# Kernel optimization log

Hardware: AMD Instinct MI355X
Metric: run time of the kernel (lower is better)

The kernel has to match this reference:

```python
import jax, jax.numpy as jnp
import numpy as np
from math import sqrt

D_MODEL = 1024
D_HEAD = 128
TAU = 30.0
B, L = 8, 2048


def setup_inputs() -> dict:
    key = jax.random.key(0)
    k1, k2, k3, k4 = jax.random.split(key, 4)
    x = jax.random.normal(k1, (B, L, D_MODEL), dtype=jnp.float32)
    attention_mask = jnp.ones((B, L), dtype=jnp.int32)
    W_Q = jax.random.normal(k2, (D_HEAD, D_MODEL), dtype=jnp.float32)
    W_K = jax.random.normal(k3, (D_HEAD, D_MODEL), dtype=jnp.float32)
    W_V = jax.random.normal(k4, (D_HEAD, D_MODEL), dtype=jnp.float32)
    return {"input": x, "attention_mask": attention_mask, "W_Q": W_Q, "W_K": W_K, "W_V": W_V}


def reference(input, attention_mask, W_Q, W_K, W_V):
    # Single-head projections: [B, L, d_head]
    Q = input @ W_Q.T
    K = input @ W_K.T
    V = input @ W_V.T
    # Scaled scores: [B, L, L]
    S = jnp.einsum("bqd,bkd->bqk", Q, K) / sqrt(D_HEAD)
    # tanh soft-capping (mode == 'tanh-clipped')
    S = TAU * jnp.tanh(S)
    l = input.shape[1]
    # causal mask: strictly upper triangle -> -inf
    causal = jnp.triu(jnp.ones((l, l), dtype=bool), k=1)
    S = jnp.where(causal[None, :, :], -jnp.inf, S)
    # padding mask on keys: [B, 1, L]
    S = jnp.where(attention_mask[:, None, :] == 0, -jnp.inf, S)
    Attn = jax.nn.softmax(S, axis=-1)
    return Attn @ V
```

## Files before the change

### kernel.cpp

```cpp
#include <hip/hip_runtime.h>
#include <hip/hip_bf16.h>

#define BATCH  8
#define SEQ    2048
#define DMODEL 1024
#define DHEAD  128

typedef __attribute__((ext_vector_type(4))) float f32x4;
typedef __attribute__((ext_vector_type(4))) float f4;
typedef _Float16 f16;
typedef __attribute__((ext_vector_type(8))) _Float16 f16x8;
typedef __attribute__((ext_vector_type(8))) __bf16 bf16x8;
typedef __attribute__((ext_vector_type(16))) unsigned short u16x16;

__device__ __forceinline__ unsigned short f2bf(float f) {
    unsigned u = __builtin_bit_cast(unsigned, f);
    u += 0x7fffu + ((u >> 16) & 1u);
    return (unsigned short)(u >> 16);
}

#if __has_builtin(__builtin_amdgcn_exp2f)
#define EXP2(x) __builtin_amdgcn_exp2f(x)
#else
#define EXP2(x) exp2f(x)
#endif

__device__ __forceinline__ float fast_rcp(float x) {
#if __has_builtin(__builtin_amdgcn_rcpf)
    return __builtin_amdgcn_rcpf(x);
#else
    return 1.0f / x;
#endif
}

__global__ __launch_bounds__(256) void wsplit_kernel(
    const float* __restrict__ WQ, const float* __restrict__ WK,
    const float* __restrict__ WV, f16* __restrict__ Wsp)
{
    const int gid = blockIdx.x * 256 + threadIdx.x;
    const int row = gid & 127;
    const int hi  = (gid >> 7) & 3;
    const int ks  = (gid >> 9) & 31;
    const int mat = gid >> 14;
    const float* W = (mat < 2) ? WQ : (mat < 4) ? WK : WV;
    const float* src = W + (size_t)row * DMODEL + ks * 32 + hi * 8;
    f4 v0 = *(const f4*)src, v1 = *(const f4*)(src + 4);
    const bool lopart = (mat == 1 || mat == 3);
    f16x8 o;
    #pragma unroll
    for (int j = 0; j < 4; ++j) {
        f16 h0 = (f16)v0[j], h1 = (f16)v1[j];
        o[j]     = lopart ? (f16)(v0[j] - (float)h0) : h0;
        o[j + 4] = lopart ? (f16)(v1[j] - (float)h1) : h1;
    }
    *reinterpret_cast<f16x8*>(Wsp + (size_t)gid * 8) = o;
}

__global__ __launch_bounds__(256, 2) void proj_kernel(
    const float* __restrict__ x, const f16* __restrict__ Wsp,
    f16* __restrict__ Qh, f16* __restrict__ Ql,
    f16* __restrict__ Kh, f16* __restrict__ Kl,
    unsigned short* __restrict__ Vtb)
{
    __shared__ f16 Ax[2][2][4][8][17][8];

    const int tid  = threadIdx.x;
    const int lane = tid & 63;
    const int w    = tid >> 6;
    const int lo   = lane & 15;
    const int hi   = lane >> 4;
    const int m0   = blockIdx.x * 64;
    const int bn   = blockIdx.y;
    const int fi   = hi * 128 + bn * 64 + w * 16 + lo;

    const int xrow = tid >> 2;
    const int xg   = tid & 3;
    const int xrb  = xrow >> 4, xro = xrow & 15;

    f32x4 accQ[4] = {}, accK[4] = {}, accV[4] = {};

    const float* xbase = x + (size_t)(m0 + xrow) * DMODEL + xg * 8;
    const f16*   wbase = Wsp + (size_t)fi * 8;

    f4 rx0, rx1, rx2, rx3;
    auto loadX = [&](int ks2) {
        const float* p = xbase + ks2 * 64;
        rx0 = *(const f4*)(p);
        rx1 = *(const f4*)(p + 4);
        rx2 = *(const f4*)(p + 32);
        rx3 = *(const f4*)(p + 36);
    };
    auto cvt8 = [](f4 v0, f4 v1, f16x8& h8, f16x8& l8) {
        #pragma unroll
        for (int j = 0; j < 4; ++j) {
            f16 h0 = (f16)v0[j]; h8[j]     = h0; l8[j]     = (f16)(v0[j] - (float)h0);
            f16 h1 = (f16)v1[j]; h8[j + 4] = h1; l8[j + 4] = (f16)(v1[j] - (float)h1);
        }
    };
    auto writeX = [&](int buf) {
        f16x8 h8, l8;
        cvt8(rx0, rx1, h8, l8);
        *reinterpret_cast<f16x8*>(&Ax[buf][0][xrb][xg][xro][0]) = h8;
        *reinterpret_cast<f16x8*>(&Ax[buf][1][xrb][xg][xro][0]) = l8;
        cvt8(rx2, rx3, h8, l8);
        *reinterpret_cast<f16x8*>(&Ax[buf][0][xrb][xg + 4][xro][0]) = h8;
        *reinterpret_cast<f16x8*>(&Ax[buf][1][xrb][xg + 4][xro][0]) = l8;
    };

    loadX(0);
    writeX(0);
    __syncthreads();

    for (int ks2 = 0; ks2 < 16; ++ks2) {
        const int cur = ks2 & 1;
        if (ks2 < 15) loadX(ks2 + 1);

        f16x8 W10[10];
        #pragma unroll
        for (int kk = 0; kk < 2; ++kk)
            #pragma unroll
            for (int m = 0; m < 5; ++m)
                W10[kk * 5 + m] = *reinterpret_cast<const f16x8*>(
                    wbase + (size_t)(m * 32 + ks2 * 2 + kk) * 4096);

        #pragma unroll
        for (int kk = 0; kk < 2; ++kk) {
            const f16x8* Wc = &W10[kk * 5];
            #pragma unroll
            for (int rb = 0; rb < 4; ++rb) {
                f16x8 ah = *reinterpret_cast<const f16x8*>(&Ax[cur][0][rb][kk * 4 + hi][lo][0]);
                f16x8 al = *reinterpret_cast<const f16x8*>(&Ax[cur][1][rb][kk * 4 + hi][lo][0]);
                accQ[rb] = __builtin_amdgcn_mfma_f32_16x16x32_f16(ah, Wc[0], accQ[rb], 0, 0, 0);
                accQ[rb] = __builtin_amdgcn_mfma_f32_16x16x32_f16(ah, Wc[1], accQ[rb], 0, 0, 0);
                accQ[rb] = __builtin_amdgcn_mfma_f32_16x16x32_f16(al, Wc[0], accQ[rb], 0, 0, 0);
                accK[rb] = __builtin_amdgcn_mfma_f32_16x16x32_f16(ah, Wc[2], accK[rb], 0, 0, 0);
                accK[rb] = __builtin_amdgcn_mfma_f32_16x16x32_f16(ah, Wc[3], accK[rb], 0, 0, 0);
                accK[rb] = __builtin_amdgcn_mfma_f32_16x16x32_f16(al, Wc[2], accK[rb], 0, 0, 0);
                accV[rb] = __builtin_amdgcn_mfma_f32_16x16x32_f16(ah, Wc[4], accV[rb], 0, 0, 0);
            }
        }
        if (ks2 < 15) writeX(cur ^ 1);
        __syncthreads();
    }

    #pragma unroll
    for (int rb = 0; rb < 4; ++rb)
        #pragma unroll
        for (int r = 0; r < 4; ++r) {
            const int m = m0 + rb * 16 + hi * 4 + r;
            const int n = bn * 64 + w * 16 + lo;
            const size_t idx = (size_t)m * DHEAD + n;
            float vq = accQ[rb][r];
            f16 hq = (f16)vq;
            Qh[idx] = hq; Ql[idx] = (f16)(vq - (float)hq);
            float vk = accK[rb][r];
            f16 hk = (f16)vk;
            Kh[idx] = hk; Kl[idx] = (f16)(vk - (float)hk);
            const int bb = m >> 11, l = m & 2047;
            Vtb[((size_t)bb * DHEAD + n) * SEQ + l] = f2bf(accV[rb][r]);
        }
}

#define PART_STRIDE 8256
__global__ __launch_bounds__(512) void attn_kernel(
    const f16* __restrict__ Qh, const f16* __restrict__ Ql,
    const f16* __restrict__ Kh, const f16* __restrict__ Kl,
    const unsigned short* __restrict__ Vtb, const int* __restrict__ mask,
    float* __restrict__ part)
{
    __shared__ f16 Khs[64][136];
    __shared__ f16 Kls[64][136];
    __shared__ unsigned short Vs[128][72];
    __shared__ int Ms[64];
    __shared__ unsigned short Plds[8][16][40];

    const int tid  = threadIdx.x;
    const int lane = tid & 63;
    const int w    = tid >> 6;
    const int lo   = lane & 15;
    const int hi   = lane >> 4;
    const int wq   = w & 3;
    const int wk   = w >> 2;
    const int b    = blockIdx.x;
    const int qs   = 31 - (int)blockIdx.y;
    const int z    = blockIdx.z;
    const int qrow = qs * 64 + wq * 16;

    const float c2p = 0.25506061907448296f;
    const float c1  = -86.561702453337804f;

    f16x8 qh[4], ql[4];
    {
        const size_t off = ((size_t)(b * SEQ + qrow + lo)) * DHEAD + hi * 8;
        #pragma unroll
        for (int c = 0; c < 4; ++c) {
            qh[c] = *reinterpret_cast<const f16x8*>(Qh + off + c * 32);
            ql[c] = *reinterpret_cast<const f16x8*>(Ql + off + c * 32);
        }
    }

    const int krow = tid >> 3;
    const int kcol = (tid & 7) * 16;
    const int vrow = tid >> 2;
    const int vcol = (tid & 3) * 16;

    f16x8  rKh0, rKh1, rKl0, rKl1;
    u16x16 rV;
    int    rM = 0;

    auto load_tile = [&](int kb) {
        const size_t koff = ((size_t)(b * SEQ + kb + krow)) * DHEAD + kcol;
        rKh0 = *reinterpret_cast<const f16x8*>(Kh + koff);
        rKh1 = *reinterpret_cast<const f16x8*>(Kh + koff + 8);
        rKl0 = *reinterpret_cast<const f16x8*>(Kl + koff);
        rKl1 = *reinterpret_cast<const f16x8*>(Kl + koff + 8);
        rV   = *reinterpret_cast<const u16x16*>(Vtb + ((size_t)b * DHEAD + vrow) * SEQ + kb + vcol);
        if (tid < 64) rM = mask[b * SEQ + kb + tid];
    };
    auto write_tile = [&]() {
        *reinterpret_cast<f16x8*>(&Khs[krow][kcol])     = rKh0;
        *reinterpret_cast<f16x8*>(&Khs[krow][kcol + 8]) = rKh1;
        *reinterpret_cast<f16x8*>(&Kls[krow][kcol])     = rKl0;
        *reinterpret_cast<f16x8*>(&Kls[krow][kcol + 8]) = rKl1;
        *reinterpret_cast<u16x16*>(&Vs[vrow][vcol]) = rV;
        if (tid < 64) Ms[tid] = rM;
    };

    load_tile(z * 64);
    write_tile();
    if (z + 2 <= qs) load_tile((z + 2) * 64);
    __syncthreads();

    f32x4 acc[8] = {};
    float rs[4] = {0.f, 0.f, 0.f, 0.f};

    for (int it = z; it <= qs; it += 2) {
        const int kb = it * 64 + wk * 32;
        if (kb <= qrow + 15) {
            #pragma unroll
            for (int h = 0; h < 2; ++h) {
                f32x4 s = {};
                #pragma unroll
                for (int c = 0; c < 4; ++c) {
                    f16x8 fkh = *reinterpret_cast<const f16x8*>(&Khs[wk * 32 + h * 16 + lo][c * 32 + hi * 8]);
                    f16x8 fkl = *reinterpret_cast<const f16x8*>(&Kls[wk * 32 + h * 16 + lo][c * 32 + hi * 8]);
                    s = __builtin_amdgcn_mfma_f32_16x16x32_f16(qh[c], fkh, s, 0, 0, 0);
                    s = __builtin_amdgcn_mfma_f32_16x16x32_f16(qh[c], fkl, s, 0, 0, 0);
                    s = __builtin_amdgcn_mfma_f32_16x16x32_f16(ql[c], fkh, s, 0, 0, 0);
                }
                const int key = kb + h * 16 + lo;
                const int mk  = Ms[wk * 32 + h * 16 + lo];
                #pragma unroll
                for (int r = 0; r < 4; ++r) {
                    const int q = qrow + hi * 4 + r;
                    float t = EXP2(s[r] * c2p);
                    float p = EXP2(c1 * fast_rcp(t + 1.0f));
                    p = (key <= q && mk != 0) ? p : 0.0f;
                    rs[r] += p;
                    Plds[w][hi * 4 + r][h * 16 + lo] = f2bf(p);
                }
            }
            bf16x8 pa = *reinterpret_cast<const bf16x8*>(&Plds[w][lo][hi * 8]);
            #pragma unroll
            for (int dt = 0; dt < 8; ++dt) {
                bf16x8 vf = *reinterpret_cast<const bf16x8*>(&Vs[dt * 16 + lo][wk * 32 + hi * 8]);
                acc[dt] = __builtin_amdgcn_mfma_f32_16x16x32_bf16(pa, vf, acc[dt], 0, 0, 0);
            }
        }

        __syncthreads();
        if (it + 2 <= qs) {
            write_tile();
            if (it + 4 <= qs) load_tile((it + 4) * 64);
        }
        __syncthreads();
    }

    float* red = (float*)&Khs[0][0];
    if (wk == 1) {
        float* dst = red + ((size_t)wq * 64 + lane) * 36;
        #pragma unroll
        for (int dt = 0; dt < 8; ++dt)
            #pragma unroll
            for (int r = 0; r < 4; ++r) dst[dt * 4 + r] = acc[dt][r];
        #pragma unroll
        for (int r = 0; r < 4; ++r) dst[32 + r] = rs[r];
    }
    __syncthreads();
    if (wk == 0) {
        const float* src = red + ((size_t)wq * 64 + lane) * 36;
        #pragma unroll
        for (int dt = 0; dt < 8; ++dt)
            #pragma unroll
            for (int r = 0; r < 4; ++r) acc[dt][r] += src[dt * 4 + r];
        float rsum[4];
        #pragma unroll
        for (int r = 0; r < 4; ++r) {
            float v = rs[r] + src[32 + r];
            v += __shfl_xor(v, 1);
            v += __shfl_xor(v, 2);
            v += __shfl_xor(v, 4);
            v += __shfl_xor(v, 8);
            rsum[r] = v;
        }
        float* P = part + (((size_t)b * 32 + qs) * 2 + z) * PART_STRIDE;
        #pragma unroll
        for (int dt = 0; dt < 8; ++dt)
            #pragma unroll
            for (int r = 0; r < 4; ++r)
                P[(wq * 16 + hi * 4 + r) * 128 + dt * 16 + lo] = acc[dt][r];
        if (lo == 0)
            #pragma unroll
            for (int r = 0; r < 4; ++r)
                P[8192 + wq * 16 + hi * 4 + r] = rsum[r];
    }
}

__global__ __launch_bounds__(256) void merge_kernel(
    const float* __restrict__ part, float* __restrict__ out)
{
    const int gid = blockIdx.x * 256 + threadIdx.x;
    const int col = (gid & 31) * 4;
    const int q   = gid >> 5;
    const int b   = q >> 11, l = q & 2047;
    const int qs  = l >> 6, row = l & 63;
    const float* P0 = part + (((size_t)b * 32 + qs) * 2) * PART_STRIDE;
    const float* P1 = P0 + PART_STRIDE;
    f4 a0 = *(const f4*)(P0 + row * 128 + col);
    f4 a1 = *(const f4*)(P1 + row * 128 + col);
    float inv = fast_rcp(P0[8192 + row] + P1[8192 + row]);
    f4 o;
    #pragma unroll
    for (int j = 0; j < 4; ++j) o[j] = (a0[j] + a1[j]) * inv;
    *(f4*)(out + (size_t)q * 128 + col) = o;
}

extern "C" void kernel_launch(void* const* d_in, const int* in_sizes, int n_in,
                              void* d_out, int out_size, void* d_ws, size_t ws_size,
                              hipStream_t stream) {
    const float* x   = (const float*)d_in[0];
    const int*   msk = (const int*)d_in[1];
    const float* WQ  = (const float*)d_in[2];
    const float* WK  = (const float*)d_in[3];
    const float* WV  = (const float*)d_in[4];
    float* out = (float*)d_out;

    const size_t NE = (size_t)BATCH * SEQ * DHEAD;
    f16* Qh = (f16*)d_ws;
    f16* Ql = Qh + NE;
    f16* Kh = Ql + NE;
    f16* Kl = Kh + NE;
    unsigned short* Vtb = (unsigned short*)(Kl + NE);
    f16* Wsp = (f16*)(Vtb + NE);
    float* part = (float*)(Wsp + (size_t)5 * 32 * 4096);

    wsplit_kernel<<<320, 256, 0, stream>>>(WQ, WK, WV, Wsp);
    proj_kernel<<<dim3(BATCH * SEQ / 64, 2), 256, 0, stream>>>(x, Wsp, Qh, Ql, Kh, Kl, Vtb);
    attn_kernel<<<dim3(BATCH, 32, 2), 512, 0, stream>>>(Qh, Ql, Kh, Kl, Vtb, msk, part);
    merge_kernel<<<2048, 256, 0, stream>>>(part, out);
}
```

Baseline: 87.84 us.

## Split attention keys across more blocks with smaller 256-thread workgroups

The attention kernel drops the intra-block two-way key split and its shared-memory reduction. It uses 256-thread blocks of 4 waves that each walk 32-key tiles, and raises the split-K factor across blocks to 4 when the workspace is large enough. The merge kernel now sums NZ partials. This adds parallelism and removes the block-level reduction, at the cost of more partial-result traffic and more Q reloads per block.

New measurement: 95.26 us. 8.4% more time.

```diff
diff --git a/kernel.cpp b/kernel.cpp
--- a/kernel.cpp
+++ b/kernel.cpp
@@ -162,29 +162,29 @@
 }
 
 #define PART_STRIDE 8256
-__global__ __launch_bounds__(512) void attn_kernel(
+__global__ __launch_bounds__(256) void attn_kernel(
     const f16* __restrict__ Qh, const f16* __restrict__ Ql,
     const f16* __restrict__ Kh, const f16* __restrict__ Kl,
     const unsigned short* __restrict__ Vtb, const int* __restrict__ mask,
     float* __restrict__ part)
 {
-    __shared__ f16 Khs[64][136];
-    __shared__ f16 Kls[64][136];
-    __shared__ unsigned short Vs[128][72];
-    __shared__ int Ms[64];
-    __shared__ unsigned short Plds[8][16][40];
+    __shared__ f16 Khs[32][136];
+    __shared__ f16 Kls[32][136];
+    __shared__ unsigned short Vs[128][40];
+    __shared__ int Ms[32];
+    __shared__ unsigned short Plds[4][16][40];
 
     const int tid  = threadIdx.x;
     const int lane = tid & 63;
     const int w    = tid >> 6;
     const int lo   = lane & 15;
     const int hi   = lane >> 4;
-    const int wq   = w & 3;
-    const int wk   = w >> 2;
     const int b    = blockIdx.x;
     const int qs   = 31 - (int)blockIdx.y;
     const int z    = blockIdx.z;
-    const int qrow = qs * 64 + wq * 16;
+    const int NZ   = gridDim.z;
+    const int qrow = qs * 64 + w * 16;
+    const int ntiles = qs * 2 + 2;
 
     const float c2p = 0.25506061907448296f;
     const float c1  = -86.561702453337804f;
@@ -201,8 +201,8 @@
 
     const int krow = tid >> 3;
     const int kcol = (tid & 7) * 16;
-    const int vrow = tid >> 2;
-    const int vcol = (tid & 3) * 16;
+    const int vrow = tid >> 1;
+    const int vcol = (tid & 1) * 16;
 
     f16x8  rKh0, rKh1, rKl0, rKl1;
     u16x16 rV;
@@ -215,7 +215,7 @@
         rKl0 = *reinterpret_cast<const f16x8*>(Kl + koff);
         rKl1 = *reinterpret_cast<const f16x8*>(Kl + koff + 8);
         rV   = *reinterpret_cast<const u16x16*>(Vtb + ((size_t)b * DHEAD + vrow) * SEQ + kb + vcol);
-        if (tid < 64) rM = mask[b * SEQ + kb + tid];
+        if (tid < 32) rM = mask[b * SEQ + kb + tid];
     };
     auto write_tile = [&]() {
         *reinterpret_cast<f16x8*>(&Khs[krow][kcol])     = rKh0;
@@ -223,33 +223,33 @@
         *reinterpret_cast<f16x8*>(&Kls[krow][kcol])     = rKl0;
         *reinterpret_cast<f16x8*>(&Kls[krow][kcol + 8]) = rKl1;
         *reinterpret_cast<u16x16*>(&Vs[vrow][vcol]) = rV;
-        if (tid < 64) Ms[tid] = rM;
-    };
-
-    load_tile(z * 64);
+        if (tid < 32) Ms[tid] = rM;
+    };
+
+    load_tile(z * 32);
     write_tile();
-    if (z + 2 <= qs) load_tile((z + 2) * 64);
+    if (z + NZ < ntiles) load_tile((z + NZ) * 32);
     __syncthreads();
 
     f32x4 acc[8] = {};
     float rs[4] = {0.f, 0.f, 0.f, 0.f};
 
-    for (int it = z; it <= qs; it += 2) {
-        const int kb = it * 64 + wk * 32;
+    for (int it = z; it < ntiles; it += NZ) {
+        const int kb = it * 32;
         if (kb <= qrow + 15) {
             #pragma unroll
             for (int h = 0; h < 2; ++h) {
                 f32x4 s = {};
                 #pragma unroll
                 for (int c = 0; c < 4; ++c) {
-                    f16x8 fkh = *reinterpret_cast<const f16x8*>(&Khs[wk * 32 + h * 16 + lo][c * 32 + hi * 8]);
-                    f16x8 fkl = *reinterpret_cast<const f16x8*>(&Kls[wk * 32 + h * 16 + lo][c * 32 + hi * 8]);
+                    f16x8 fkh = *reinterpret_cast<const f16x8*>(&Khs[h * 16 + lo][c * 32 + hi * 8]);
+                    f16x8 fkl = *reinterpret_cast<const f16x8*>(&Kls[h * 16 + lo][c * 32 + hi * 8]);
                     s = __builtin_amdgcn_mfma_f32_16x16x32_f16(qh[c], fkh, s, 0, 0, 0);
                     s = __builtin_amdgcn_mfma_f32_16x16x32_f16(qh[c], fkl, s, 0, 0, 0);
                     s = __builtin_amdgcn_mfma_f32_16x16x32_f16(ql[c], fkh, s, 0, 0, 0);
                 }
                 const int key = kb + h * 16 + lo;
-                const int mk  = Ms[wk * 32 + h * 16 + lo];
+                const int mk  = Ms[h * 16 + lo];
                 #pragma unroll
                 for (int r = 0; r < 4; ++r) {
                     const int q = qrow + hi * 4 + r;
@@ -263,75 +263,63 @@
             bf16x8 pa = *reinterpret_cast<const bf16x8*>(&Plds[w][lo][hi * 8]);
             #pragma unroll
             for (int dt = 0; dt < 8; ++dt) {
-                bf16x8 vf = *reinterpret_cast<const bf16x8*>(&Vs[dt * 16 + lo][wk * 32 + hi * 8]);
+                bf16x8 vf = *reinterpret_cast<const bf16x8*>(&Vs[dt * 16 + lo][hi * 8]);
                 acc[dt] = __builtin_amdgcn_mfma_f32_16x16x32_bf16(pa, vf, acc[dt], 0, 0, 0);
             }
         }
 
         __syncthreads();
-        if (it + 2 <= qs) {
+        if (it + NZ < ntiles) {
             write_tile();
-            if (it + 4 <= qs) load_tile((it + 4) * 64);
+            if (it + 2 * NZ < ntiles) load_tile((it + 2 * NZ) * 32);
         }
         __syncthreads();
     }
 
-    float* red = (float*)&Khs[0][0];
-    if (wk == 1) {
-        float* dst = red + ((size_t)wq * 64 + lane) * 36;
-        #pragma unroll
-        for (int dt = 0; dt < 8; ++dt)
-            #pragma unroll
-            for (int r = 0; r < 4; ++r) dst[dt * 4 + r] = acc[dt][r];
-        #pragma unroll
-        for (int r = 0; r < 4; ++r) dst[32 + r] = rs[r];
-    }
-    __syncthreads();
-    if (wk == 0) {
-        const float* src = red + ((size_t)wq * 64 + lane) * 36;
-        #pragma unroll
-        for (int dt = 0; dt < 8; ++dt)
-            #pragma unroll
-            for (int r = 0; r < 4; ++r) acc[dt][r] += src[dt * 4 + r];
-        float rsum[4];
-        #pragma unroll
-        for (int r = 0; r < 4; ++r) {
-            float v = rs[r] + src[32 + r];
-            v += __shfl_xor(v, 1);
-            v += __shfl_xor(v, 2);
-            v += __shfl_xor(v, 4);
-            v += __shfl_xor(v, 8);
-            rsum[r] = v;
-        }
-        float* P = part + (((size_t)b * 32 + qs) * 2 + z) * PART_STRIDE;
-        #pragma unroll
-        for (int dt = 0; dt < 8; ++dt)
-            #pragma unroll
-            for (int r = 0; r < 4; ++r)
-                P[(wq * 16 + hi * 4 + r) * 128 + dt * 16 + lo] = acc[dt][r];
-        if (lo == 0)
-            #pragma unroll
-            for (int r = 0; r < 4; ++r)
-                P[8192 + wq * 16 + hi * 4 + r] = rsum[r];
-    }
+    float rsum[4];
+    #pragma unroll
+    for (int r = 0; r < 4; ++r) {
+        float v = rs[r];
+        v += __shfl_xor(v, 1);
+        v += __shfl_xor(v, 2);
+        v += __shfl_xor(v, 4);
+        v += __shfl_xor(v, 8);
+        rsum[r] = v;
+    }
+    float* P = part + (((size_t)b * 32 + qs) * NZ + z) * PART_STRIDE;
+    #pragma unroll
+    for (int dt = 0; dt < 8; ++dt)
+        #pragma unroll
+        for (int r = 0; r < 4; ++r)
+            P[(w * 16 + hi * 4 + r) * 128 + dt * 16 + lo] = acc[dt][r];
+    if (lo == 0)
+        #pragma unroll
+        for (int r = 0; r < 4; ++r)
+            P[8192 + w * 16 + hi * 4 + r] = rsum[r];
 }
 
 __global__ __launch_bounds__(256) void merge_kernel(
-    const float* __restrict__ part, float* __restrict__ out)
+    const float* __restrict__ part, float* __restrict__ out, int NZ)
 {
     const int gid = blockIdx.x * 256 + threadIdx.x;
     const int col = (gid & 31) * 4;
     const int q   = gid >> 5;
     const int b   = q >> 11, l = q & 2047;
     const int qs  = l >> 6, row = l & 63;
-    const float* P0 = part + (((size_t)b * 32 + qs) * 2) * PART_STRIDE;
-    const float* P1 = P0 + PART_STRIDE;
-    f4 a0 = *(const f4*)(P0 + row * 128 + col);
-    f4 a1 = *(const f4*)(P1 + row * 128 + col);
-    float inv = fast_rcp(P0[8192 + row] + P1[8192 + row]);
+    const float* P0 = part + (((size_t)b * 32 + qs) * NZ) * PART_STRIDE;
+    f4 a = {};
+    float den = 0.f;
+    for (int zz = 0; zz < NZ; ++zz) {
+        const float* P = P0 + (size_t)zz * PART_STRIDE;
+        f4 av = *(const f4*)(P + row * 128 + col);
+        #pragma unroll
+        for (int j = 0; j < 4; ++j) a[j] += av[j];
+        den += P[8192 + row];
+    }
+    float inv = fast_rcp(den);
     f4 o;
     #pragma unroll
-    for (int j = 0; j < 4; ++j) o[j] = (a0[j] + a1[j]) * inv;
+    for (int j = 0; j < 4; ++j) o[j] = a[j] * inv;
     *(f4*)(out + (size_t)q * 128 + col) = o;
 }
 
@@ -354,8 +342,12 @@
     f16* Wsp = (f16*)(Vtb + NE);
     float* part = (float*)(Wsp + (size_t)5 * 32 * 4096);
 
+    const size_t base = (size_t)5 * NE * 2 + (size_t)5 * 32 * 4096 * 2;
+    const size_t part4 = (size_t)BATCH * 32 * 4 * PART_STRIDE * 4;
+    const int NZ = (ws_size >= base + part4) ? 4 : 2;
+
     wsplit_kernel<<<320, 256, 0, stream>>>(WQ, WK, WV, Wsp);
     proj_kernel<<<dim3(BATCH * SEQ / 64, 2), 256, 0, stream>>>(x, Wsp, Qh, Ql, Kh, Kl, Vtb);
-    attn_kernel<<<dim3(BATCH, 32, 2), 512, 0, stream>>>(Qh, Ql, Kh, Kl, Vtb, msk, part);
-    merge_kernel<<<2048, 256, 0, stream>>>(part, out);
-}
+    attn_kernel<<<dim3(BATCH, 32, NZ), 256, 0, stream>>>(Qh, Ql, Kh, Kl, Vtb, msk, part);
+    merge_kernel<<<2048, 256, 0, stream>>>(part, out, NZ);
+}
```
